# Kernel tuning notes

Hardware: AMD Instinct MI355X
Metric: run time of the kernel (lower is better)

## Reference

```python
import jax, jax.numpy as jnp
import numpy as np

N_NODES = 50000


def gcn_conv(x, edge_index, W, b, n_nodes):
    # PyG GCNConv: h = D^{-1/2} (A + I) D^{-1/2} (x @ W) + b
    loops = jnp.arange(n_nodes, dtype=edge_index.dtype)
    src = jnp.concatenate([edge_index[0], loops])
    dst = jnp.concatenate([edge_index[1], loops])
    deg = jax.ops.segment_sum(jnp.ones_like(dst, dtype=x.dtype), dst,
                              num_segments=n_nodes)
    dinv = jnp.where(deg > 0, jax.lax.rsqrt(deg), 0.0)
    norm = dinv[src] * dinv[dst]                      # [E+N]
    h = x @ W                                          # [N, out]
    msg = h[src] * norm[:, None]                       # gather + scale
    out = jax.ops.segment_sum(msg, dst, num_segments=n_nodes)
    return out + b


def setup_inputs() -> dict:
    key = jax.random.key(0)
    ks = jax.random.split(key, 8)
    in_c, hid_c, out_c = 256, 128, 64
    x = jax.random.normal(ks[0], (N_NODES, in_c), dtype=jnp.float32)
    edge_index = jax.random.randint(ks[1], (2, 800000), 0, N_NODES, dtype=jnp.int64)
    pos_edge_index = jax.random.randint(ks[2], (2, 200000), 0, N_NODES, dtype=jnp.int64)
    neg_edge_index = jax.random.randint(ks[3], (2, 200000), 0, N_NES if False else N_NODES, dtype=jnp.int64)
    W1 = jax.random.normal(ks[4], (in_c, hid_c), dtype=jnp.float32) / np.sqrt(in_c)
    b1 = jnp.zeros((hid_c,), dtype=jnp.float32)
    W2 = jax.random.normal(ks[5], (hid_c, out_c), dtype=jnp.float32) / np.sqrt(hid_c)
    b2 = jnp.zeros((out_c,), dtype=jnp.float32)
    return {"x": x, "edge_index": edge_index, "pos_edge_index": pos_edge_index,
            "neg_edge_index": neg_edge_index, "W1": W1, "b1": b1, "W2": W2, "b2": b2}


def reference(x, edge_index, pos_edge_index, neg_edge_index, W1, b1, W2, b2):
    n = x.shape[0]
    h = jax.nn.relu(gcn_conv(x, edge_index, W1, b1, n))
    z = gcn_conv(h, edge_index, W2, b2, n)             # [N, out_c]
    ei = jnp.concatenate([pos_edge_index, neg_edge_index], axis=-1)
    logits = jnp.sum(z[ei[0]] * z[ei[1]], axis=-1)     # [E_pos + E_neg]
    return logits
```

## Files before the change

### kernel.cpp

```cpp
#include <hip/hip_runtime.h>
#include <stdint.h>

constexpr int N_NODES = 50000;
constexpr int E_EDGES = 800000;
constexpr int E_PAIR  = 200000;
constexpr int C_IN    = 256;
constexpr int C_HID   = 128;
constexpr int C_OUT   = 64;
constexpr int SLOT    = 64;

constexpr int NBUCK = 196;
constexpr int BCAP  = 4608;
constexpr int CHUNK = 2048;

typedef __attribute__((ext_vector_type(8))) short bf8_t;
typedef __attribute__((ext_vector_type(4))) float f32x4;

__device__ inline void bf_split(float v, uint32_t& hi16, uint32_t& lo16) {
    union { float f; uint32_t u; } c; c.f = v;
    hi16 = c.u >> 16;
    union { uint32_t u; float f; } h; h.u = hi16 << 16;
    float r = v - h.f;
    union { float f; uint32_t u; } rr; rr.f = r;
    lo16 = rr.u >> 16;
}

__device__ inline uint16_t f2bf(float f) {
    union { float f; uint32_t u; } c; c.f = f;
    uint32_t u = c.u + 0x7fff + ((c.u >> 16) & 1);
    return (uint16_t)(u >> 16);
}
__device__ inline uint32_t pack2bf(float a, float b) {
    union { float f; uint32_t u; } ca, cb; ca.f = a; cb.f = b;
    uint32_t ua = ca.u + 0x7fff + ((ca.u >> 16) & 1);
    uint32_t ub = cb.u + 0x7fff + ((cb.u >> 16) & 1);
    return (ua >> 16) | ((ub >> 16) << 16);
}
__device__ inline void acc_bf8(float* a, uint4 v) {
    const uint32_t p[4] = {v.x, v.y, v.z, v.w};
#pragma unroll
    for (int i = 0; i < 4; ++i) {
        union { uint32_t u; float f; } lo, hi;
        lo.u = p[i] << 16; hi.u = p[i] & 0xffff0000u;
        a[2 * i]     += lo.f;
        a[2 * i + 1] += hi.f;
    }
}
__device__ inline float dot_bf8(uint4 a, uint4 b) {
    const uint32_t pa[4] = {a.x, a.y, a.z, a.w};
    const uint32_t pb[4] = {b.x, b.y, b.z, b.w};
    float v = 0.f;
#pragma unroll
    for (int i = 0; i < 4; ++i) {
        union { uint32_t u; float f; } al, ah, bl, bh;
        al.u = pa[i] << 16; ah.u = pa[i] & 0xffff0000u;
        bl.u = pb[i] << 16; bh.u = pb[i] & 0xffff0000u;
        v += al.f * bl.f + ah.f * bh.f;
    }
    return v;
}

template<int N>
__device__ inline int wswz_idx(int k, int n) {
    int c = k >> 5, kq = (k >> 3) & 3, kk = k & 7, ct = n >> 4, nn = n & 15;
    return (((c * (N / 16) + ct) * 4 + kq) * 16 + nn) * 8 + kk;
}

__global__ __launch_bounds__(256) void prep_kernel(
        const float* __restrict__ W1, const float* __restrict__ W2,
        uint16_t* __restrict__ s1, uint16_t* __restrict__ s2,
        int* __restrict__ gcur) {
    int id = blockIdx.x * 256 + threadIdx.x;
    if (id < NBUCK) gcur[id] = 0;
    if (id < C_IN * C_HID) {
        uint32_t h, l; bf_split(W1[id], h, l);
        int idx = wswz_idx<C_HID>(id / C_HID, id & (C_HID - 1));
        s1[idx]                 = (uint16_t)h;
        s1[C_IN * C_HID + idx]  = (uint16_t)l;
    } else if (id < C_IN * C_HID + C_HID * C_OUT) {
        int id2 = id - C_IN * C_HID;
        uint32_t h, l; bf_split(W2[id2], h, l);
        int idx = wswz_idx<C_OUT>(id2 / C_OUT, id2 & (C_OUT - 1));
        s2[idx]                 = (uint16_t)h;
        s2[C_HID * C_OUT + idx] = (uint16_t)l;
    }
}

__global__ __launch_bounds__(256) void binA_kernel(
        const int* __restrict__ src, const int* __restrict__ dst,
        int* __restrict__ gcur, uint32_t* __restrict__ ebuf) {
    __shared__ int cnt[NBUCK], loc[NBUCK], lim[NBUCK], abase[NBUCK], wcur[NBUCK];
    __shared__ uint32_t stag[CHUNK];
    __shared__ uint8_t  bof[CHUNK];

    const int t  = threadIdx.x;
    const int e0 = blockIdx.x * CHUNK;
    const int n  = min(CHUNK, E_EDGES - e0);

    for (int b = t; b < NBUCK; b += 256) cnt[b] = 0;
    __syncthreads();

    uint32_t pk[CHUNK / 256]; int bk[CHUNK / 256];
    int ne = 0;
    for (int j = t; j < n; j += 256) {
        int d = dst[e0 + j], s = src[e0 + j];
        int b = d >> 8;
        pk[ne] = ((uint32_t)(d & 255) << 16) | (uint32_t)s;
        bk[ne] = b;
        atomicAdd(&cnt[b], 1);
        ++ne;
    }
    __syncthreads();
    if (t == 0) {
        int run = 0;
        for (int b = 0; b < NBUCK; ++b) { loc[b] = run; run += cnt[b]; }
    }
    __syncthreads();
    for (int b = t; b < NBUCK; b += 256) {
        int base = atomicAdd(&gcur[b], cnt[b]);
        int room = BCAP - base; if (room < 0) room = 0;
        lim[b]   = loc[b] + room;
        abase[b] = b * BCAP + base - loc[b];
        wcur[b]  = loc[b];
    }
    __syncthreads();
#pragma unroll
    for (int i = 0; i < CHUNK / 256; ++i) {
        if (i < ne) {
            int p = atomicAdd(&wcur[bk[i]], 1);
            stag[p] = pk[i];
            bof[p]  = (uint8_t)bk[i];
        }
    }
    __syncthreads();
    for (int j = t; j < n; j += 256) {
        int b = bof[j];
        if (j < lim[b]) ebuf[abase[b] + j] = stag[j];
    }
}

__global__ __launch_bounds__(256) void binB_kernel(
        const int* __restrict__ gcur, const uint32_t* __restrict__ ebuf,
        uint16_t* __restrict__ col2, int* __restrict__ degc,
        float* __restrict__ dinv) {
    __shared__ int cur[256];
    const int t = threadIdx.x;
    const int b = blockIdx.x;
    cur[t] = 0;
    __syncthreads();

    int cn = gcur[b]; if (cn > BCAP) cn = BCAP;
    const uint32_t* eb = ebuf + (size_t)b * BCAP;
    const size_t nbase = (size_t)b << 8;

    int j = t;
    for (; j + 3 * 256 < cn; j += 4 * 256) {
        uint32_t v0 = eb[j], v1 = eb[j + 256], v2 = eb[j + 512], v3 = eb[j + 768];
        int p0 = atomicAdd(&cur[v0 >> 16], 1);
        int p1 = atomicAdd(&cur[v1 >> 16], 1);
        int p2 = atomicAdd(&cur[v2 >> 16], 1);
        int p3 = atomicAdd(&cur[v3 >> 16], 1);
        if (p0 < SLOT) col2[((nbase + (v0 >> 16)) << 6) + p0] = (uint16_t)(v0 & 0xffff);
        if (p1 < SLOT) col2[((nbase + (v1 >> 16)) << 6) + p1] = (uint16_t)(v1 & 0xffff);
        if (p2 < SLOT) col2[((nbase + (v2 >> 16)) << 6) + p2] = (uint16_t)(v2 & 0xffff);
        if (p3 < SLOT) col2[((nbase + (v3 >> 16)) << 6) + p3] = (uint16_t)(v3 & 0xffff);
    }
    for (; j < cn; j += 256) {
        uint32_t v = eb[j];
        int p = atomicAdd(&cur[v >> 16], 1);
        if (p < SLOT) col2[((nbase + (v >> 16)) << 6) + p] = (uint16_t)(v & 0xffff);
    }
    __syncthreads();
    int node = (int)nbase + t;
    if (node < N_NODES) {
        int dg = cur[t];
        degc[node] = dg;
        dinv[node] = rsqrtf((float)dg + 1.0f);
    }
}

template<int K, int N>
__global__ __launch_bounds__(256, 3) void gemm_mfma_kernel(
        const float* __restrict__ A, const uint16_t* __restrict__ Bswz,
        const float* __restrict__ dinv, uint16_t* __restrict__ out, int M) {
    constexpr int BM = 64, BK = 32;
    constexpr int CT   = N / 32;
    constexpr int NSUB = N / 16;
    constexpr int ABYTES = BM * BK * 2;
    constexpr int BBYTES = NSUB * 1024;
    __shared__ char sm[2 * ABYTES + 2 * BBYTES];
    char* As_hi = sm;
    char* As_lo = sm + ABYTES;
    char* Bs_hi = sm + 2 * ABYTES;
    char* Bs_lo = sm + 2 * ABYTES + BBYTES;

    const int t    = threadIdx.x;
    const int lane = t & 63;
    const int w    = t >> 6;
    const int wrow = w & 1, wcol = w >> 1;
    const int m0   = blockIdx.x * BM;

    const int sr = t >> 2, skq = t & 3;
    int arow = m0 + sr; if (arow > M - 1) arow = M - 1;
    const float* aptr = A + (size_t)arow * K + skq * 8;
    const int aslot = ((sr >> 4) * 64 + skq * 16 + (sr & 15)) * 16;

    f32x4 acc[2][CT];
#pragma unroll
    for (int rt = 0; rt < 2; ++rt)
#pragma unroll
        for (int ct = 0; ct < CT; ++ct) {
            f32x4 z = {0.f, 0.f, 0.f, 0.f};
            acc[rt][ct] = z;
        }

    const uint4* gh = (const uint4*)Bswz;
    const uint4* gl = (const uint4*)(Bswz + (size_t)K * N);

    constexpr int NCH = K / BK;
#pragma unroll 1
    for (int c = 0; c < NCH; ++c) {
        float4 v0 = *(const float4*)(aptr + c * BK);
        float4 v1 = *(const float4*)(aptr + c * BK + 4);
        uint4 bh0, bl0, bh1, bl1;
        {
            const uint4* ch = gh + (size_t)c * (BBYTES / 16);
            const uint4* cl = gl + (size_t)c * (BBYTES / 16);
            bh0 = ch[t]; bl0 = cl[t];
            if constexpr (NSUB == 8) { bh1 = ch[t + 256]; bl1 = cl[t + 256]; }
        }
        __syncthreads();
        {
            float e[8] = {v0.x, v0.y, v0.z, v0.w, v1.x, v1.y, v1.z, v1.w};
            uint32_t hp[4], lp[4];
#pragma unroll
            for (int j = 0; j < 4; ++j) {
                uint32_t h0, l0, h1, l1;
                bf_split(e[2 * j],     h0, l0);
                bf_split(e[2 * j + 1], h1, l1);
                hp[j] = h0 | (h1 << 16);
                lp[j] = l0 | (l1 << 16);
            }
            *(uint4*)(As_hi + aslot) = make_uint4(hp[0], hp[1], hp[2], hp[3]);
            *(uint4*)(As_lo + aslot) = make_uint4(lp[0], lp[1], lp[2], lp[3]);
        }
        *(uint4*)(Bs_hi + t * 16) = bh0;
        *(uint4*)(Bs_lo + t * 16) = bl0;
        if constexpr (NSUB == 8) {
            *(uint4*)(Bs_hi + (t + 256) * 16) = bh1;
            *(uint4*)(Bs_lo + (t + 256) * 16) = bl1;
        }
        __syncthreads();
        bf8_t Ah[2], Al[2];
#pragma unroll
        for (int rt = 0; rt < 2; ++rt) {
            int st = wrow * 2 + rt;
            Ah[rt] = *(const bf8_t*)(As_hi + st * 1024 + lane * 16);
            Al[rt] = *(const bf8_t*)(As_lo + st * 1024 + lane * 16);
        }
#pragma unroll
        for (int ct = 0; ct < CT; ++ct) {
            int cg = wcol * CT + ct;
            bf8_t Bh = *(const bf8_t*)(Bs_hi + cg * 1024 + lane * 16);
            bf8_t Bl = *(const bf8_t*)(Bs_lo + cg * 1024 + lane * 16);
#pragma unroll
            for (int rt = 0; rt < 2; ++rt) {
                acc[rt][ct] = __builtin_amdgcn_mfma_f32_16x16x32_bf16(Ah[rt], Bh, acc[rt][ct], 0, 0, 0);
                acc[rt][ct] = __builtin_amdgcn_mfma_f32_16x16x32_bf16(Ah[rt], Bl, acc[rt][ct], 0, 0, 0);
                acc[rt][ct] = __builtin_amdgcn_mfma_f32_16x16x32_bf16(Al[rt], Bh, acc[rt][ct], 0, 0, 0);
            }
        }
    }

#pragma unroll
    for (int rt = 0; rt < 2; ++rt) {
        int rowbase = m0 + wrow * 32 + rt * 16 + (lane >> 4) * 4;
#pragma unroll
        for (int ct = 0; ct < CT; ++ct) {
            int n = (wcol * CT + ct) * 16 + (lane & 15);
#pragma unroll
            for (int r = 0; r < 4; ++r) {
                int m = rowbase + r;
                if (m < M) out[(size_t)m * N + n] = f2bf(acc[rt][ct][r] * dinv[m]);
            }
        }
    }
}

__global__ __launch_bounds__(256) void gather_gemm_kernel(
        const uint16_t* __restrict__ col2, const int* __restrict__ degc,
        const uint16_t* __restrict__ h0s, const float* __restrict__ dinv,
        const float* __restrict__ bias, const uint16_t* __restrict__ B2swz,
        uint16_t* __restrict__ z0s) {
    __shared__ uint4 hlds[256];
    const int t    = threadIdx.x;
    const int lane = t & 63;
    const int w    = t >> 6;
    const int sub  = lane >> 4;
    const int l    = lane & 15;
    const int node_loc = w * 4 + sub;
    const int node = blockIdx.x * 16 + node_loc;

    int dg = degc[node]; if (dg > SLOT) dg = SLOT;
    const uint4* hs4 = (const uint4*)h0s;
    float a0[8], a1[8];
    {
        uint4 self = hs4[(size_t)node * 16 + l];
#pragma unroll
        for (int i = 0; i < 8; ++i) { a0[i] = 0.f; a1[i] = 0.f; }
        acc_bf8(a0, self);
    }
    const int base = node * SLOT;
    for (int c = 0; c * 16 < dg; ++c) {
        int cnt = dg - c * 16; if (cnt > 16) cnt = 16;
        int cv = (l < cnt) ? (int)col2[base + c * 16 + l] : 0;
        int j = 0;
        for (; j + 8 <= cnt; j += 8) {
            int s0 = __shfl(cv, sub * 16 + j,     64);
            int s1 = __shfl(cv, sub * 16 + j + 1, 64);
            int s2 = __shfl(cv, sub * 16 + j + 2, 64);
            int s3 = __shfl(cv, sub * 16 + j + 3, 64);
            int s4 = __shfl(cv, sub * 16 + j + 4, 64);
            int s5 = __shfl(cv, sub * 16 + j + 5, 64);
            int s6 = __shfl(cv, sub * 16 + j + 6, 64);
            int s7 = __shfl(cv, sub * 16 + j + 7, 64);
            uint4 v0 = hs4[(size_t)s0 * 16 + l];
            uint4 v1 = hs4[(size_t)s1 * 16 + l];
            uint4 v2 = hs4[(size_t)s2 * 16 + l];
            uint4 v3 = hs4[(size_t)s3 * 16 + l];
            uint4 v4 = hs4[(size_t)s4 * 16 + l];
            uint4 v5 = hs4[(size_t)s5 * 16 + l];
            uint4 v6 = hs4[(size_t)s6 * 16 + l];
            uint4 v7 = hs4[(size_t)s7 * 16 + l];
            acc_bf8(a0, v0); acc_bf8(a1, v1);
            acc_bf8(a0, v2); acc_bf8(a1, v3);
            acc_bf8(a0, v4); acc_bf8(a1, v5);
            acc_bf8(a0, v6); acc_bf8(a1, v7);
        }
        for (; j + 4 <= cnt; j += 4) {
            int s0 = __shfl(cv, sub * 16 + j,     64);
            int s1 = __shfl(cv, sub * 16 + j + 1, 64);
            int s2 = __shfl(cv, sub * 16 + j + 2, 64);
            int s3 = __shfl(cv, sub * 16 + j + 3, 64);
            uint4 v0 = hs4[(size_t)s0 * 16 + l];
            uint4 v1 = hs4[(size_t)s1 * 16 + l];
            uint4 v2 = hs4[(size_t)s2 * 16 + l];
            uint4 v3 = hs4[(size_t)s3 * 16 + l];
            acc_bf8(a0, v0); acc_bf8(a1, v1);
            acc_bf8(a0, v2); acc_bf8(a1, v3);
        }
        for (; j < cnt; ++j) {
            int s = __shfl(cv, sub * 16 + j, 64);
            uint4 v = hs4[(size_t)s * 16 + l];
            acc_bf8(a0, v);
        }
    }
    {
        const float dn = dinv[node];
        float4 bb0 = ((const float4*)bias)[2 * l];
        float4 bb1 = ((const float4*)bias)[2 * l + 1];
        float o[8];
        o[0] = fmaxf((a0[0] + a1[0]) * dn + bb0.x, 0.f);
        o[1] = fmaxf((a0[1] + a1[1]) * dn + bb0.y, 0.f);
        o[2] = fmaxf((a0[2] + a1[2]) * dn + bb0.z, 0.f);
        o[3] = fmaxf((a0[3] + a1[3]) * dn + bb0.w, 0.f);
        o[4] = fmaxf((a0[4] + a1[4]) * dn + bb1.x, 0.f);
        o[5] = fmaxf((a0[5] + a1[5]) * dn + bb1.y, 0.f);
        o[6] = fmaxf((a0[6] + a1[6]) * dn + bb1.z, 0.f);
        o[7] = fmaxf((a0[7] + a1[7]) * dn + bb1.w, 0.f);
        hlds[l * 16 + node_loc] = make_uint4(
            pack2bf(o[0], o[1]), pack2bf(o[2], o[3]),
            pack2bf(o[4], o[5]), pack2bf(o[6], o[7]));
    }
    __syncthreads();

    f32x4 acc = {0.f, 0.f, 0.f, 0.f};
    const char* hb = (const char*)hlds;
#pragma unroll
    for (int c = 0; c < 4; ++c) {
        bf8_t Af = *(const bf8_t*)(hb + c * 1024 + lane * 16);
        const uint16_t* bp = B2swz + (c * 4 + w) * 512 + lane * 8;
        bf8_t Bh = *(const bf8_t*)bp;
        bf8_t Bl = *(const bf8_t*)(bp + C_HID * C_OUT);
        acc = __builtin_amdgcn_mfma_f32_16x16x32_bf16(Af, Bh, acc, 0, 0, 0);
        acc = __builtin_amdgcn_mfma_f32_16x16x32_bf16(Af, Bl, acc, 0, 0, 0);
    }
    const int colg = w * 16 + (lane & 15);
    const int rowb = blockIdx.x * 16 + (lane >> 4) * 4;
#pragma unroll
    for (int r = 0; r < 4; ++r) {
        int m = rowb + r;
        z0s[(size_t)m * C_OUT + colg] = f2bf(acc[r] * dinv[m]);
    }
}

template<int F, bool RELU>
__global__ __launch_bounds__(256) void gather_kernel(
        const uint16_t* __restrict__ col2, const int* __restrict__ degc,
        const uint16_t* __restrict__ hs, const float* __restrict__ dinv,
        const float* __restrict__ bias, uint16_t* __restrict__ out) {
    constexpr int LPN = F / 8;
    constexpr int NPW = 64 / LPN;
    const int lane = threadIdx.x & 63;
    const int sub  = lane / LPN;
    const int l    = lane % LPN;
    const int node = blockIdx.x * (4 * NPW) + (threadIdx.x >> 6) * NPW + sub;
    if (node >= N_NODES) return;

    int dg = degc[node]; if (dg > SLOT) dg = SLOT;
    const uint4* hs4 = (const uint4*)hs;

    float a0[8], a1[8];
    {
        uint4 self = hs4[(size_t)node * LPN + l];
#pragma unroll
        for (int i = 0; i < 8; ++i) { a0[i] = 0.f; a1[i] = 0.f; }
        acc_bf8(a0, self);
    }
    const int base = node * SLOT;

    for (int c = 0; c * LPN < dg; ++c) {
        int cnt = dg - c * LPN; if (cnt > LPN) cnt = LPN;
        int cv = (l < cnt) ? (int)col2[base + c * LPN + l] : 0;
        int j = 0;
        for (; j + 8 <= cnt; j += 8) {
            int s0 = __shfl(cv, sub * LPN + j,     64);
            int s1 = __shfl(cv, sub * LPN + j + 1, 64);
            int s2 = __shfl(cv, sub * LPN + j + 2, 64);
            int s3 = __shfl(cv, sub * LPN + j + 3, 64);
            int s4 = __shfl(cv, sub * LPN + j + 4, 64);
            int s5 = __shfl(cv, sub * LPN + j + 5, 64);
            int s6 = __shfl(cv, sub * LPN + j + 6, 64);
            int s7 = __shfl(cv, sub * LPN + j + 7, 64);
            uint4 v0 = hs4[(size_t)s0 * LPN + l];
            uint4 v1 = hs4[(size_t)s1 * LPN + l];
            uint4 v2 = hs4[(size_t)s2 * LPN + l];
            uint4 v3 = hs4[(size_t)s3 * LPN + l];
            uint4 v4 = hs4[(size_t)s4 * LPN + l];
            uint4 v5 = hs4[(size_t)s5 * LPN + l];
            uint4 v6 = hs4[(size_t)s6 * LPN + l];
            uint4 v7 = hs4[(size_t)s7 * LPN + l];
            acc_bf8(a0, v0); acc_bf8(a1, v1);
            acc_bf8(a0, v2); acc_bf8(a1, v3);
            acc_bf8(a0, v4); acc_bf8(a1, v5);
            acc_bf8(a0, v6); acc_bf8(a1, v7);
        }
        for (; j + 4 <= cnt; j += 4) {
            int s0 = __shfl(cv, sub * LPN + j,     64);
            int s1 = __shfl(cv, sub * LPN + j + 1, 64);
            int s2 = __shfl(cv, sub * LPN + j + 2, 64);
            int s3 = __shfl(cv, sub * LPN + j + 3, 64);
            uint4 v0 = hs4[(size_t)s0 * LPN + l];
            uint4 v1 = hs4[(size_t)s1 * LPN + l];
            uint4 v2 = hs4[(size_t)s2 * LPN + l];
            uint4 v3 = hs4[(size_t)s3 * LPN + l];
            acc_bf8(a0, v0); acc_bf8(a1, v1);
            acc_bf8(a0, v2); acc_bf8(a1, v3);
        }
        for (; j < cnt; ++j) {
            int s = __shfl(cv, sub * LPN + j, 64);
            uint4 v = hs4[(size_t)s * LPN + l];
            acc_bf8(a0, v);
        }
    }

    const float dn = dinv[node];
    float4 bb0 = ((const float4*)bias)[2 * l];
    float4 bb1 = ((const float4*)bias)[2 * l + 1];
    float o[8];
    o[0] = (a0[0] + a1[0]) * dn + bb0.x;
    o[1] = (a0[1] + a1[1]) * dn + bb0.y;
    o[2] = (a0[2] + a1[2]) * dn + bb0.z;
    o[3] = (a0[3] + a1[3]) * dn + bb0.w;
    o[4] = (a0[4] + a1[4]) * dn + bb1.x;
    o[5] = (a0[5] + a1[5]) * dn + bb1.y;
    o[6] = (a0[6] + a1[6]) * dn + bb1.z;
    o[7] = (a0[7] + a1[7]) * dn + bb1.w;
    if (RELU) {
#pragma unroll
        for (int i = 0; i < 8; ++i) o[i] = fmaxf(o[i], 0.f);
    }
    uint4 res = make_uint4(pack2bf(o[0], o[1]), pack2bf(o[2], o[3]),
                           pack2bf(o[4], o[5]), pack2bf(o[6], o[7]));
    ((uint4*)out)[(size_t)node * LPN + l] = res;
}

__global__ __launch_bounds__(256) void logits_kernel(
        const int* __restrict__ pos, const int* __restrict__ neg,
        const uint16_t* __restrict__ z, float* __restrict__ out) {
    const int t = threadIdx.x;
    const int l = t & 7;
    const int g = (blockIdx.x * 256 + t) >> 3;
    const int e0 = 2 * g;
    if (e0 >= 2 * E_PAIR) return;
    int s0, d0, s1, d1;
    if (e0 < E_PAIR) { s0 = pos[e0];          d0 = pos[E_PAIR + e0]; }
    else             { s0 = neg[e0 - E_PAIR]; d0 = neg[e0];          }
    int e1 = e0 + 1;
    if (e1 < E_PAIR) { s1 = pos[e1];          d1 = pos[E_PAIR + e1]; }
    else             { s1 = neg[e1 - E_PAIR]; d1 = neg[e1];          }
    const uint4* z4 = (const uint4*)z;
    uint4 ua0 = z4[(size_t)s0 * 8 + l];
    uint4 ub0 = z4[(size_t)d0 * 8 + l];
    uint4 ua1 = z4[(size_t)s1 * 8 + l];
    uint4 ub1 = z4[(size_t)d1 * 8 + l];
    float v0 = dot_bf8(ua0, ub0);
    float v1 = dot_bf8(ua1, ub1);
    v0 += __shfl_xor(v0, 1, 64); v1 += __shfl_xor(v1, 1, 64);
    v0 += __shfl_xor(v0, 2, 64); v1 += __shfl_xor(v1, 2, 64);
    v0 += __shfl_xor(v0, 4, 64); v1 += __shfl_xor(v1, 4, 64);
    if (l == 0) { out[e0] = v0; out[e1] = v1; }
}

extern "C" void kernel_launch(void* const* d_in, const int* in_sizes, int n_in,
                              void* d_out, int out_size, void* d_ws, size_t ws_size,
                              hipStream_t stream) {
    const float* x   = (const float*)d_in[0];
    const int*   ei  = (const int*)d_in[1];
    const int*   pos = (const int*)d_in[2];
    const int*   neg = (const int*)d_in[3];
    const float* W1  = (const float*)d_in[4];
    const float* b1  = (const float*)d_in[5];
    const float* W2  = (const float*)d_in[6];
    const float* b2  = (const float*)d_in[7];
    float* out = (float*)d_out;

    const int* src = ei;
    const int* dst = ei + E_EDGES;

    char* ws = (char*)d_ws;
    int*      degc  = (int*)ws;
    float*    dinv  = (float*)(ws + 200704);
    uint16_t* col2  = (uint16_t*)(ws + 401408);
    int*      gcur  = (int*)(ws + 6801408);
    uint16_t* B1swz = (uint16_t*)(ws + 6802432);
    uint16_t* B2swz = (uint16_t*)(ws + 6933504);
    uint16_t* h0s   = (uint16_t*)(ws + 6966272);
    uint16_t* z0s   = (uint16_t*)(ws + 32566272);
    uint16_t* zbuf  = (uint16_t*)(ws + 38966272);
    uint32_t* ebuf  = (uint32_t*)(ws + 45366272);

    prep_kernel<<<(C_IN * C_HID + C_HID * C_OUT + 255) / 256, 256, 0, stream>>>(
        W1, W2, B1swz, B2swz, gcur);

    binA_kernel<<<(E_EDGES + CHUNK - 1) / CHUNK, 256, 0, stream>>>(src, dst, gcur, ebuf);
    binB_kernel<<<NBUCK, 256, 0, stream>>>(gcur, ebuf, col2, degc, dinv);

    gemm_mfma_kernel<C_IN, C_HID><<<(N_NODES + 63) / 64, 256, 0, stream>>>(
        x, B1swz, dinv, h0s, N_NODES);

    gather_gemm_kernel<<<N_NODES / 16, 256, 0, stream>>>(
        col2, degc, h0s, dinv, b1, B2swz, z0s);

    gather_kernel<C_OUT, false><<<(N_NODES + 31) / 32, 256, 0, stream>>>(
        col2, degc, z0s, dinv, b2, zbuf);

    logits_kernel<<<(E_PAIR * 8 + 255) / 256, 256, 0, stream>>>(pos, neg, zbuf, out);
}
```

Baseline: 205.4 us.

## Merge CSR build and first GEMM into one launch, move source dinv scaling to gather

The second binning kernel (slot fill, degree and dinv) and the first MFMA GEMM now run as one launch with a block-index split. The GEMM no longer depends on dinv, so it can run concurrently with graph construction. To make that possible, the source-side dinv scaling moved from the GEMM epilogue into the first gather, which now loads dinv per neighbour and multiplies each gathered row. The cost is an extra scattered dinv load and multiplies per edge in the gather, plus a longer combined kernel whose two block types do unequal work.

```diff
diff --git a/kernel.cpp b/kernel.cpp
--- a/kernel.cpp
+++ b/kernel.cpp
@@ -12,6 +12,7 @@
 constexpr int NBUCK = 196;
 constexpr int BCAP  = 4608;
 constexpr int CHUNK = 2048;
+constexpr int GEMM1_BLOCKS = (N_NODES + 63) / 64;
 
 typedef __attribute__((ext_vector_type(8))) short bf8_t;
 typedef __attribute__((ext_vector_type(4))) float f32x4;
@@ -44,6 +45,16 @@
         lo.u = p[i] << 16; hi.u = p[i] & 0xffff0000u;
         a[2 * i]     += lo.f;
         a[2 * i + 1] += hi.f;
+    }
+}
+__device__ inline void acc_bf8s(float* a, uint4 v, float s) {
+    const uint32_t p[4] = {v.x, v.y, v.z, v.w};
+#pragma unroll
+    for (int i = 0; i < 4; ++i) {
+        union { uint32_t u; float f; } lo, hi;
+        lo.u = p[i] << 16; hi.u = p[i] & 0xffff0000u;
+        a[2 * i]     += lo.f * s;
+        a[2 * i + 1] += hi.f * s;
     }
 }
 __device__ inline float dot_bf8(uint4 a, uint4 b) {
@@ -139,66 +150,69 @@
     }
 }
 
-__global__ __launch_bounds__(256) void binB_kernel(
+__global__ __launch_bounds__(256, 3) void build_gemm_kernel(
         const int* __restrict__ gcur, const uint32_t* __restrict__ ebuf,
         uint16_t* __restrict__ col2, int* __restrict__ degc,
-        float* __restrict__ dinv) {
-    __shared__ int cur[256];
-    const int t = threadIdx.x;
-    const int b = blockIdx.x;
-    cur[t] = 0;
-    __syncthreads();
-
-    int cn = gcur[b]; if (cn > BCAP) cn = BCAP;
-    const uint32_t* eb = ebuf + (size_t)b * BCAP;
-    const size_t nbase = (size_t)b << 8;
-
-    int j = t;
-    for (; j + 3 * 256 < cn; j += 4 * 256) {
-        uint32_t v0 = eb[j], v1 = eb[j + 256], v2 = eb[j + 512], v3 = eb[j + 768];
-        int p0 = atomicAdd(&cur[v0 >> 16], 1);
-        int p1 = atomicAdd(&cur[v1 >> 16], 1);
-        int p2 = atomicAdd(&cur[v2 >> 16], 1);
-        int p3 = atomicAdd(&cur[v3 >> 16], 1);
-        if (p0 < SLOT) col2[((nbase + (v0 >> 16)) << 6) + p0] = (uint16_t)(v0 & 0xffff);
-        if (p1 < SLOT) col2[((nbase + (v1 >> 16)) << 6) + p1] = (uint16_t)(v1 & 0xffff);
-        if (p2 < SLOT) col2[((nbase + (v2 >> 16)) << 6) + p2] = (uint16_t)(v2 & 0xffff);
-        if (p3 < SLOT) col2[((nbase + (v3 >> 16)) << 6) + p3] = (uint16_t)(v3 & 0xffff);
-    }
-    for (; j < cn; j += 256) {
-        uint32_t v = eb[j];
-        int p = atomicAdd(&cur[v >> 16], 1);
-        if (p < SLOT) col2[((nbase + (v >> 16)) << 6) + p] = (uint16_t)(v & 0xffff);
-    }
-    __syncthreads();
-    int node = (int)nbase + t;
-    if (node < N_NODES) {
-        int dg = cur[t];
-        degc[node] = dg;
-        dinv[node] = rsqrtf((float)dg + 1.0f);
-    }
-}
-
-template<int K, int N>
-__global__ __launch_bounds__(256, 3) void gemm_mfma_kernel(
+        float* __restrict__ dinv,
         const float* __restrict__ A, const uint16_t* __restrict__ Bswz,
-        const float* __restrict__ dinv, uint16_t* __restrict__ out, int M) {
+        uint16_t* __restrict__ out) {
+    constexpr int K = C_IN, N = C_HID;
     constexpr int BM = 64, BK = 32;
     constexpr int CT   = N / 32;
     constexpr int NSUB = N / 16;
     constexpr int ABYTES = BM * BK * 2;
     constexpr int BBYTES = NSUB * 1024;
     __shared__ char sm[2 * ABYTES + 2 * BBYTES];
+
+    const int t = threadIdx.x;
+
+    if (blockIdx.x < NBUCK) {
+        int* cur = (int*)sm;
+        const int b = blockIdx.x;
+        cur[t] = 0;
+        __syncthreads();
+
+        int cn = gcur[b]; if (cn > BCAP) cn = BCAP;
+        const uint32_t* eb = ebuf + (size_t)b * BCAP;
+        const size_t nbase = (size_t)b << 8;
+
+        int j = t;
+        for (; j + 3 * 256 < cn; j += 4 * 256) {
+            uint32_t v0 = eb[j], v1 = eb[j + 256], v2 = eb[j + 512], v3 = eb[j + 768];
+            int p0 = atomicAdd(&cur[v0 >> 16], 1);
+            int p1 = atomicAdd(&cur[v1 >> 16], 1);
+            int p2 = atomicAdd(&cur[v2 >> 16], 1);
+            int p3 = atomicAdd(&cur[v3 >> 16], 1);
+            if (p0 < SLOT) col2[((nbase + (v0 >> 16)) << 6) + p0] = (uint16_t)(v0 & 0xffff);
+            if (p1 < SLOT) col2[((nbase + (v1 >> 16)) << 6) + p1] = (uint16_t)(v1 & 0xffff);
+            if (p2 < SLOT) col2[((nbase + (v2 >> 16)) << 6) + p2] = (uint16_t)(v2 & 0xffff);
+            if (p3 < SLOT) col2[((nbase + (v3 >> 16)) << 6) + p3] = (uint16_t)(v3 & 0xffff);
+        }
+        for (; j < cn; j += 256) {
+            uint32_t v = eb[j];
+            int p = atomicAdd(&cur[v >> 16], 1);
+            if (p < SLOT) col2[((nbase + (v >> 16)) << 6) + p] = (uint16_t)(v & 0xffff);
+        }
+        __syncthreads();
+        int node = (int)nbase + t;
+        if (node < N_NODES) {
+            int dg = cur[t];
+            degc[node] = dg;
+            dinv[node] = rsqrtf((float)dg + 1.0f);
+        }
+        return;
+    }
+
     char* As_hi = sm;
     char* As_lo = sm + ABYTES;
     char* Bs_hi = sm + 2 * ABYTES;
     char* Bs_lo = sm + 2 * ABYTES + BBYTES;
 
-    const int t    = threadIdx.x;
     const int lane = t & 63;
     const int w    = t >> 6;
     const int wrow = w & 1, wcol = w >> 1;
-    const int m0   = blockIdx.x * BM;
+    const int m0   = (blockIdx.x - NBUCK) * BM;
+    const int M    = N_NODES;
 
     const int sr = t >> 2, skq = t & 3;
     int arow = m0 + sr; if (arow > M - 1) arow = M - 1;
@@ -227,7 +241,7 @@
             const uint4* ch = gh + (size_t)c * (BBYTES / 16);
             const uint4* cl = gl + (size_t)c * (BBYTES / 16);
             bh0 = ch[t]; bl0 = cl[t];
-            if constexpr (NSUB == 8) { bh1 = ch[t + 256]; bl1 = cl[t + 256]; }
+            bh1 = ch[t + 256]; bl1 = cl[t + 256];
         }
         __syncthreads();
         {
@@ -246,10 +260,8 @@
         }
         *(uint4*)(Bs_hi + t * 16) = bh0;
         *(uint4*)(Bs_lo + t * 16) = bl0;
-        if constexpr (NSUB == 8) {
-            *(uint4*)(Bs_hi + (t + 256) * 16) = bh1;
-            *(uint4*)(Bs_lo + (t + 256) * 16) = bl1;
-        }
+        *(uint4*)(Bs_hi + (t + 256) * 16) = bh1;
+        *(uint4*)(Bs_lo + (t + 256) * 16) = bl1;
         __syncthreads();
         bf8_t Ah[2], Al[2];
 #pragma unroll
@@ -281,7 +293,7 @@
 #pragma unroll
             for (int r = 0; r < 4; ++r) {
                 int m = rowbase + r;
-                if (m < M) out[(size_t)m * N + n] = f2bf(acc[rt][ct][r] * dinv[m]);
+                if (m < M) out[(size_t)m * N + n] = f2bf(acc[rt][ct][r]);
             }
         }
     }
@@ -289,7 +301,7 @@
 
 __global__ __launch_bounds__(256) void gather_gemm_kernel(
         const uint16_t* __restrict__ col2, const int* __restrict__ degc,
-        const uint16_t* __restrict__ h0s, const float* __restrict__ dinv,
+        const uint16_t* __restrict__ h0u, const float* __restrict__ dinv,
         const float* __restrict__ bias, const uint16_t* __restrict__ B2swz,
         uint16_t* __restrict__ z0s) {
     __shared__ uint4 hlds[256];
@@ -302,13 +314,14 @@
     const int node = blockIdx.x * 16 + node_loc;
 
     int dg = degc[node]; if (dg > SLOT) dg = SLOT;
-    const uint4* hs4 = (const uint4*)h0s;
+    const float dn = dinv[node];
+    const uint4* hs4 = (const uint4*)h0u;
     float a0[8], a1[8];
     {
         uint4 self = hs4[(size_t)node * 16 + l];
 #pragma unroll
         for (int i = 0; i < 8; ++i) { a0[i] = 0.f; a1[i] = 0.f; }
-        acc_bf8(a0, self);
+        acc_bf8s(a0, self, dn);
     }
     const int base = node * SLOT;
     for (int c = 0; c * 16 < dg; ++c) {
@@ -332,10 +345,12 @@
             uint4 v5 = hs4[(size_t)s5 * 16 + l];
             uint4 v6 = hs4[(size_t)s6 * 16 + l];
             uint4 v7 = hs4[(size_t)s7 * 16 + l];
-            acc_bf8(a0, v0); acc_bf8(a1, v1);
-            acc_bf8(a0, v2); acc_bf8(a1, v3);
-            acc_bf8(a0, v4); acc_bf8(a1, v5);
-            acc_bf8(a0, v6); acc_bf8(a1, v7);
+            float d0 = dinv[s0], d1 = dinv[s1], d2 = dinv[s2], d3 = dinv[s3];
+            float d4 = dinv[s4], d5 = dinv[s5], d6 = dinv[s6], d7 = dinv[s7];
+            acc_bf8s(a0, v0, d0); acc_bf8s(a1, v1, d1);
+            acc_bf8s(a0, v2, d2); acc_bf8s(a1, v3, d3);
+            acc_bf8s(a0, v4, d4); acc_bf8s(a1, v5, d5);
+            acc_bf8s(a0, v6, d6); acc_bf8s(a1, v7, d7);
         }
         for (; j + 4 <= cnt; j += 4) {
             int s0 = __shfl(cv, sub * 16 + j,     64);
@@ -346,17 +361,17 @@
             uint4 v1 = hs4[(size_t)s1 * 16 + l];
             uint4 v2 = hs4[(size_t)s2 * 16 + l];
             uint4 v3 = hs4[(size_t)s3 * 16 + l];
-            acc_bf8(a0, v0); acc_bf8(a1, v1);
-            acc_bf8(a0, v2); acc_bf8(a1, v3);
+            float d0 = dinv[s0], d1 = dinv[s1], d2 = dinv[s2], d3 = dinv[s3];
+            acc_bf8s(a0, v0, d0); acc_bf8s(a1, v1, d1);
+            acc_bf8s(a0, v2, d2); acc_bf8s(a1, v3, d3);
         }
         for (; j < cnt; ++j) {
             int s = __shfl(cv, sub * 16 + j, 64);
             uint4 v = hs4[(size_t)s * 16 + l];
-            acc_bf8(a0, v);
+            acc_bf8s(a0, v, dinv[s]);
         }
     }
     {
-        const float dn = dinv[node];
         float4 bb0 = ((const float4*)bias)[2 * l];
         float4 bb1 = ((const float4*)bias)[2 * l + 1];
         float o[8];
@@ -535,7 +550,7 @@
     int*      gcur  = (int*)(ws + 6801408);
     uint16_t* B1swz = (uint16_t*)(ws + 6802432);
     uint16_t* B2swz = (uint16_t*)(ws + 6933504);
-    uint16_t* h0s   = (uint16_t*)(ws + 6966272);
+    uint16_t* h0u   = (uint16_t*)(ws + 6966272);
     uint16_t* z0s   = (uint16_t*)(ws + 32566272);
     uint16_t* zbuf  = (uint16_t*)(ws + 38966272);
     uint32_t* ebuf  = (uint32_t*)(ws + 45366272);
@@ -544,13 +559,12 @@
         W1, W2, B1swz, B2swz, gcur);
 
     binA_kernel<<<(E_EDGES + CHUNK - 1) / CHUNK, 256, 0, stream>>>(src, dst, gcur, ebuf);
-    binB_kernel<<<NBUCK, 256, 0, stream>>>(gcur, ebuf, col2, degc, dinv);
-
-    gemm_mfma_kernel<C_IN, C_HID><<<(N_NODES + 63) / 64, 256, 0, stream>>>(
-        x, B1swz, dinv, h0s, N_NODES);
+
+    build_gemm_kernel<<<NBUCK + GEMM1_BLOCKS, 256, 0, stream>>>(
+        gcur, ebuf, col2, degc, dinv, x, B1swz, h0u);
 
     gather_gemm_kernel<<<N_NODES / 16, 256, 0, stream>>>(
-        col2, degc, h0s, dinv, b1, B2swz, z0s);
+        col2, degc, h0u, dinv, b1, B2swz, z0s);
 
     gather_kernel<C_OUT, false><<<(N_NODES + 31) / 32, 256, 0, stream>>>(
         col2, degc, z0s, dinv, b2, zbuf);
```

Result: no change. 202.4 us (-1.5%).
